# Kernel tuning notes

Hardware: AMD Instinct MI355X
Metric: run time of the kernel (lower is better)

## Reference

```python
import jax, jax.numpy as jnp
import numpy as np

D_IN = 64   # T (condition_length)
D = 128     # latent_dim
H = 8       # num_head
N = 2       # batch of graphs
M = 512     # num_nodes
T_OBS = 5.0


def leaky(v):
    return jnp.where(v >= 0, v, 0.2 * v)


def setup_inputs() -> dict:
    key = jax.random.key(0)
    ks = jax.random.split(key, 24)
    g = lambda k, s: jax.random.normal(k, s, dtype=jnp.float32) * 0.05
    return {
        "x": jax.random.normal(ks[0], (N, M, D_IN), dtype=jnp.float32),
        # f_node: T -> 2D -> D
        "fn_w1": g(ks[1], (D_IN, 2 * D)), "fn_b1": g(ks[2], (2 * D,)),
        "fn_w2": g(ks[3], (2 * D, D)),   "fn_b2": g(ks[4], (D,)),
        # per-head K/Q/V projections, stacked over heads
        "wk": g(ks[5], (H, D, D)), "bk": g(ks[6], (H, D)),
        "wq": g(ks[7], (H, D, D)), "bq": g(ks[8], (H, D)),
        "wv": g(ks[9], (H, D, D)), "bv": g(ks[10], (H, D)),
        # f_v: H*D -> D -> D
        "fv_w1": g(ks[11], (H * D, D)), "fv_b1": g(ks[12], (D,)),
        "fv_w2": g(ks[13], (D, D)),     "fv_b2": g(ks[14], (D,)),
        # f_node2edge: 2D -> D -> 1
        "fe_w1": g(ks[15], (2 * D, D)), "fe_b1": g(ks[16], (D,)),
        "fe_w2": g(ks[17], (D, 1)),     "fe_b2": g(ks[18], (1,)),
    }


def reference(x, fn_w1, fn_b1, fn_w2, fn_b2, wk, bk, wq, bq, wv, bv,
              fv_w1, fv_b1, fv_w2, fv_b2, fe_w1, fe_b1, fe_w2, fe_b2):
    n, m, T = x.shape
    # TemporalEncoding with d_hid=1: div_term = [1.0], even col -> sin(t)
    t = jnp.linspace(0.0, T_OBS, T)
    te = jnp.sin(t)  # [T]
    # f_node
    h = jax.nn.relu((x + te) @ fn_w1 + fn_b1) @ fn_w2 + fn_b2  # [N,M,D]
    # per-head attention (sender=K_i, receiver=Q_j -> scores = K Q^T)
    K = jnp.einsum('nmd,hde->hnme', h, wk) + bk[:, None, None, :]
    Q = jnp.einsum('nmd,hde->hnme', h, wq) + bq[:, None, None, :]
    V = jnp.einsum('nmd,hde->hnme', h, wv) + bv[:, None, None, :]
    scores = jnp.einsum('hnid,hnjd->hnij', K, Q)           # [H,N,M,M]
    alpha = jax.nn.softmax(leaky(scores), axis=-1)
    att = leaky(jnp.einsum('hnij,hnjd->hnid', alpha, V))   # [H,N,M,D]
    # concat heads along feature dim (head 0 first)
    att = jnp.transpose(att, (1, 2, 0, 3)).reshape(n, m, -1)  # [N,M,H*D]
    x2 = jax.nn.relu(att @ fv_w1 + fv_b1) @ fv_w2 + fv_b2 + h  # [N,M,D]
    # pairwise node2edge FFN: pair(i,j) = concat(x2_i, x2_j)
    half = fe_w1.shape[0] // 2
    A = x2 @ fe_w1[:half]   # contribution of node i
    B = x2 @ fe_w1[half:]   # contribution of node j
    hid = jax.nn.relu(A[:, :, None, :] + B[:, None, :, :] + fe_b1)  # [N,M,M,D]
    edge = (hid @ fe_w2 + fe_b2)[..., 0] / float(m)  # [N,M,M]
    return (x2, edge)
```

## Files before the change

### kernel.cpp

```cpp
#include <hip/hip_runtime.h>

typedef unsigned short u16;
typedef unsigned int u32;
typedef __attribute__((ext_vector_type(8))) short short8;
typedef __attribute__((ext_vector_type(4))) float f32x4;

__device__ __forceinline__ u16 f2b(float f) {
  union { float f; u32 i; } v; v.f = f;
  u32 i = v.i;
  return (u16)((i + 0x7FFFu + ((i >> 16) & 1u)) >> 16);
}
__device__ __forceinline__ float lo16(u32 x) { union { u32 i; float f; } v; v.i = x << 16; return v.f; }
__device__ __forceinline__ float hi16(u32 x) { union { u32 i; float f; } v; v.i = x & 0xffff0000u; return v.f; }
__device__ __forceinline__ u32 pack2(float a, float b) { return (u32)f2b(a) | ((u32)f2b(b) << 16); }

__device__ __align__(16) float g_h[1024 * 128];
__device__ __align__(16) u16   g_hb[1024 * 128];
__device__ __align__(16) u16   g_Wt[24 * 128 * 128];
__device__ __align__(16) u16   g_w1t[128 * 1024];
__device__ __align__(16) u16   g_K[16 * 512 * 128];
__device__ __align__(16) u16   g_Q[16 * 512 * 128];
__device__ __align__(16) u16   g_V[16 * 512 * 128];
__device__ __align__(16) u16   g_Opb[512 * 64 * 128];
__device__ __align__(16) float g_ml[512 * 64 * 2];
__device__ __align__(16) float g_part8[8 * 1024 * 128];
__device__ __align__(16) float g_A[1024 * 128];
__device__ __align__(16) float g_Bm[1024 * 128];

__global__ void k_fnode(const float* __restrict__ x, const float* __restrict__ w1,
                        const float* __restrict__ b1, const float* __restrict__ w2,
                        const float* __restrict__ b2, const float* __restrict__ wk,
                        const float* __restrict__ wq, const float* __restrict__ wv,
                        const float* __restrict__ fvw1) {
  __shared__ float xr[2 * 64];
  __shared__ float hids[2 * 256];
  __shared__ float red[2048];
  int tx = threadIdx.x;
  int row0 = blockIdx.x * 2;
  if (tx < 128) {
    int r = tx >> 6, k = tx & 63;
    xr[tx] = x[(row0 + r) * 64 + k] + sinf((float)k * (5.0f / 63.0f));
  }
  {
    int base = blockIdx.x * 1024 + tx;
#pragma unroll
    for (int t = 0; t < 4; t++) {
      int idx = base + t * 256;
      if (idx < 393216) {
        int ph = idx >> 14, rem = idx & 16383, e = rem >> 7, d = rem & 127;
        int proj = ph >> 3, head = ph & 7;
        const float* W = (proj == 0) ? wk : (proj == 1) ? wq : wv;
        g_Wt[idx] = f2b(W[head * 16384 + d * 128 + e]);
      } else {
        int idx2 = idx - 393216;
        int e = idx2 >> 10, k = idx2 & 1023;
        g_w1t[idx2] = f2b(fvw1[k * 128 + e]);
      }
    }
  }
  __syncthreads();
  {
    int ks = tx >> 6, cg = tx & 63;
    float acc[2][4] = {};
#pragma unroll 4
    for (int i = 0; i < 16; i++) {
      int k = ks * 16 + i;
      float4 w4 = *(const float4*)&w1[k * 256 + cg * 4];
      float a0 = xr[k], a1 = xr[64 + k];
      acc[0][0] = fmaf(a0, w4.x, acc[0][0]); acc[0][1] = fmaf(a0, w4.y, acc[0][1]);
      acc[0][2] = fmaf(a0, w4.z, acc[0][2]); acc[0][3] = fmaf(a0, w4.w, acc[0][3]);
      acc[1][0] = fmaf(a1, w4.x, acc[1][0]); acc[1][1] = fmaf(a1, w4.y, acc[1][1]);
      acc[1][2] = fmaf(a1, w4.z, acc[1][2]); acc[1][3] = fmaf(a1, w4.w, acc[1][3]);
    }
#pragma unroll
    for (int r = 0; r < 2; r++)
      *(float4*)&red[ks * 512 + r * 256 + cg * 4] = *(float4*)acc[r];
  }
  __syncthreads();
#pragma unroll
  for (int jo = 0; jo < 2; jo++) {
    int o = jo * 256 + tx;
    float s = red[o] + red[512 + o] + red[1024 + o] + red[1536 + o];
    hids[o] = fmaxf(s + b1[o & 255], 0.0f);
  }
  __syncthreads();
  {
    int ks = tx >> 5, eg = tx & 31;
    float acc[2][4] = {};
#pragma unroll 4
    for (int i = 0; i < 32; i++) {
      int k = ks * 32 + i;
      float4 w4 = *(const float4*)&w2[k * 128 + eg * 4];
      float a0 = hids[k], a1 = hids[256 + k];
      acc[0][0] = fmaf(a0, w4.x, acc[0][0]); acc[0][1] = fmaf(a0, w4.y, acc[0][1]);
      acc[0][2] = fmaf(a0, w4.z, acc[0][2]); acc[0][3] = fmaf(a0, w4.w, acc[0][3]);
      acc[1][0] = fmaf(a1, w4.x, acc[1][0]); acc[1][1] = fmaf(a1, w4.y, acc[1][1]);
      acc[1][2] = fmaf(a1, w4.z, acc[1][2]); acc[1][3] = fmaf(a1, w4.w, acc[1][3]);
    }
    __syncthreads();
#pragma unroll
    for (int r = 0; r < 2; r++)
      *(float4*)&red[ks * 256 + r * 128 + eg * 4] = *(float4*)acc[r];
  }
  __syncthreads();
  {
    float s = 0.0f;
#pragma unroll
    for (int ks = 0; ks < 8; ks++) s += red[ks * 256 + tx];
    int r = tx >> 7, e = tx & 127;
    float v = s + b2[e];
    g_h[(row0 + r) * 128 + e] = v;
    g_hb[(row0 + r) * 128 + e] = f2b(v);
  }
}

__global__ __launch_bounds__(256) void k_kqv(
    const float* __restrict__ bk, const float* __restrict__ bq,
    const float* __restrict__ bv) {
  __shared__ u16 hs[64 * 136];
  __shared__ u16 Wt[128 * 136];
  int b = blockIdx.x, tx = threadIdx.x;
  int rt = b & 15, ph = b >> 4;
  int proj = ph >> 3, head = ph & 7;
  const float* Bb = (proj == 0) ? bk : (proj == 1) ? bq : bv;
  u16* O = (proj == 0) ? g_K : (proj == 1) ? g_Q : g_V;
  int r0 = rt * 64;
#pragma unroll
  for (int t = 0; t < 4; t++) {
    int idx = t * 256 + tx, row = idx >> 4, oct = idx & 15;
    *(uint4*)&hs[row * 136 + oct * 8] = *(const uint4*)&g_hb[(r0 + row) * 128 + oct * 8];
  }
  const u16* Wtg = g_Wt + ph * 16384;
#pragma unroll
  for (int t = 0; t < 8; t++) {
    int idx = t * 256 + tx, row = idx >> 4, oct = idx & 15;
    *(uint4*)&Wt[row * 136 + oct * 8] = *(const uint4*)&Wtg[row * 128 + oct * 8];
  }
  __syncthreads();
  int lane = tx & 63, wv_ = tx >> 6, cl = lane & 15, quad = lane >> 4;
  short8 bH[4];
#pragma unroll
  for (int kk = 0; kk < 4; kk++)
    bH[kk] = *(const short8*)&hs[(wv_ * 16 + cl) * 136 + kk * 32 + quad * 8];
  f32x4 zero = {0.0f, 0.0f, 0.0f, 0.0f};
  f32x4 acc[8];
#pragma unroll
  for (int em = 0; em < 8; em++) acc[em] = zero;
#pragma unroll
  for (int em = 0; em < 8; em++)
#pragma unroll
    for (int kk = 0; kk < 4; kk++) {
      short8 aW = *(const short8*)&Wt[(em * 16 + cl) * 136 + kk * 32 + quad * 8];
      acc[em] = __builtin_amdgcn_mfma_f32_16x16x32_bf16(aW, bH[kk], acc[em], 0, 0, 0);
    }
#pragma unroll
  for (int em = 0; em < 8; em++) {
    float4 b4 = *(const float4*)&Bb[head * 128 + em * 16 + quad * 4];
    uint2 st = make_uint2(pack2(acc[em][0] + b4.x, acc[em][1] + b4.y),
                          pack2(acc[em][2] + b4.z, acc[em][3] + b4.w));
    *(uint2*)&O[(head * 1024 + r0 + wv_ * 16 + cl) * 128 + em * 16 + quad * 4] = st;
  }
}

__global__ __launch_bounds__(256) void k_attn() {
  __shared__ u16 Ks[64 * 136];
  __shared__ u16 Qs[64 * 136];
  __shared__ u16 Vt[128 * 72];
  __shared__ u16 Pw[4 * 16 * 72];
  __shared__ float alphas[4 * 16];
  int b = blockIdx.x, tx = threadIdx.x;
  int jc = b & 3, it = (b >> 2) & 7, hn = b >> 5;
  int i0 = it * 64;
  const u16* Kp = g_K + hn * 65536;
  const u16* Qp = g_Q + hn * 65536;
  const u16* Vp = g_V + hn * 65536;
#pragma unroll
  for (int t = 0; t < 4; t++) {
    int idx = t * 256 + tx, row = idx >> 4, oct = idx & 15;
    *(uint4*)&Ks[row * 136 + oct * 8] = *(const uint4*)&Kp[(i0 + row) * 128 + oct * 8];
  }
  int lane = tx & 63, wv = tx >> 6;
  int cl = lane & 15, quad = lane >> 4;
  f32x4 zero = {0.0f, 0.0f, 0.0f, 0.0f};
  f32x4 o[8];
#pragma unroll
  for (int es = 0; es < 8; es++) o[es] = zero;
  float m_ = -1e30f, l_ = 0.0f;

  for (int jt = 0; jt < 2; jt++) {
    int j0 = jc * 128 + jt * 64;
    __syncthreads();
#pragma unroll
    for (int t = 0; t < 4; t++) {
      int idx = t * 256 + tx, row = idx >> 4, oct = idx & 15;
      *(uint4*)&Qs[row * 136 + oct * 8] = *(const uint4*)&Qp[(j0 + row) * 128 + oct * 8];
    }
    {
      int jg = (tx & 15) * 4, e8 = (tx >> 4) * 8;
      uint4 r0 = *(const uint4*)&Vp[(j0 + jg + 0) * 128 + e8];
      uint4 r1 = *(const uint4*)&Vp[(j0 + jg + 1) * 128 + e8];
      uint4 r2 = *(const uint4*)&Vp[(j0 + jg + 2) * 128 + e8];
      uint4 r3 = *(const uint4*)&Vp[(j0 + jg + 3) * 128 + e8];
      const u32* p0 = (const u32*)&r0; const u32* p1 = (const u32*)&r1;
      const u32* p2 = (const u32*)&r2; const u32* p3 = (const u32*)&r3;
#pragma unroll
      for (int c = 0; c < 8; c++) {
        int w = c >> 1, sh = (c & 1) * 16;
        u32 lo = ((p0[w] >> sh) & 0xffffu) | (((p1[w] >> sh) & 0xffffu) << 16);
        u32 hi = ((p2[w] >> sh) & 0xffffu) | (((p3[w] >> sh) & 0xffffu) << 16);
        *(uint2*)&Vt[(e8 + c) * 72 + jg] = make_uint2(lo, hi);
      }
    }
    __syncthreads();
    short8 bK[4];
#pragma unroll
    for (int kk = 0; kk < 4; kk++)
      bK[kk] = *(const short8*)&Ks[(wv * 16 + cl) * 136 + kk * 32 + quad * 8];
    f32x4 st[4];
#pragma unroll
    for (int s = 0; s < 4; s++) {
      f32x4 acc = zero;
#pragma unroll
      for (int kk = 0; kk < 4; kk++) {
        short8 aQ = *(const short8*)&Qs[(s * 16 + cl) * 136 + kk * 32 + quad * 8];
        acc = __builtin_amdgcn_mfma_f32_16x16x32_bf16(aQ, bK[kk], acc, 0, 0, 0);
      }
      st[s] = acc;
    }
    float p[4][4];
    float tm = -1e30f;
#pragma unroll
    for (int s = 0; s < 4; s++)
#pragma unroll
      for (int r = 0; r < 4; r++) {
        float v = st[s][r];
        v = fmaxf(v, 0.2f * v);
        p[s][r] = v;
        tm = fmaxf(tm, v);
      }
    tm = fmaxf(tm, __shfl_xor(tm, 16));
    tm = fmaxf(tm, __shfl_xor(tm, 32));
    float mn = fmaxf(m_, tm);
    float alpha = __expf(m_ - mn);
    m_ = mn;
    float ps = 0.0f;
#pragma unroll
    for (int s = 0; s < 4; s++)
#pragma unroll
      for (int r = 0; r < 4; r++) {
        float e = __expf(p[s][r] - mn);
        p[s][r] = e;
        ps += e;
      }
    ps += __shfl_xor(ps, 16);
    ps += __shfl_xor(ps, 32);
    l_ = l_ * alpha + ps;
#pragma unroll
    for (int s = 0; s < 4; s++) {
      uint2 w2v = make_uint2(pack2(p[s][0], p[s][1]), pack2(p[s][2], p[s][3]));
      *(uint2*)&Pw[(wv * 16 + cl) * 72 + s * 16 + quad * 4] = w2v;
    }
    if (quad == 0) alphas[wv * 16 + cl] = alpha;
    __syncthreads();
    f32x4 av = *(const f32x4*)&alphas[wv * 16 + quad * 4];
#pragma unroll
    for (int es = 0; es < 8; es++) o[es] *= av;
    short8 aP[2];
#pragma unroll
    for (int k2 = 0; k2 < 2; k2++)
      aP[k2] = *(const short8*)&Pw[(wv * 16 + cl) * 72 + k2 * 32 + quad * 8];
#pragma unroll
    for (int es = 0; es < 8; es++) {
#pragma unroll
      for (int k2 = 0; k2 < 2; k2++) {
        short8 bV = *(const short8*)&Vt[(es * 16 + cl) * 72 + k2 * 32 + quad * 8];
        o[es] = __builtin_amdgcn_mfma_f32_16x16x32_bf16(aP[k2], bV, o[es], 0, 0, 0);
      }
    }
  }
#pragma unroll
  for (int es = 0; es < 8; es++)
#pragma unroll
    for (int r = 0; r < 4; r++)
      g_Opb[(b * 64 + wv * 16 + quad * 4 + r) * 128 + es * 16 + cl] = f2b(o[es][r]);
  if (quad == 0) {
    g_ml[(b * 64 + wv * 16 + cl) * 2 + 0] = m_;
    g_ml[(b * 64 + wv * 16 + cl) * 2 + 1] = l_;
  }
}

__global__ __launch_bounds__(256) void k_fv1() {
  __shared__ u16 atts[64 * 136];
  __shared__ u16 w1t[128 * 136];
  int b = blockIdx.x, tx = threadIdx.x;
  int kc = b & 7, rt = b >> 3;
  int r0 = rt * 64, k0 = kc * 128;
  int hn = kc * 2 + (rt >> 3), it = rt & 7;
#pragma unroll
  for (int t = 0; t < 8; t++) {
    int idx = t * 256 + tx, row = idx >> 4, oct = idx & 15;
    *(uint4*)&w1t[row * 136 + oct * 8] = *(const uint4*)&g_w1t[row * 1024 + k0 + oct * 8];
  }
  {
    int row = tx >> 2, cs = (tx & 3) * 32;
    float mc[4], lc[4];
#pragma unroll
    for (int c = 0; c < 4; c++) {
      float2 ml = *(const float2*)&g_ml[((hn * 32 + it * 4 + c) * 64 + row) * 2];
      mc[c] = ml.x; lc[c] = ml.y;
    }
    float ms = fmaxf(fmaxf(mc[0], mc[1]), fmaxf(mc[2], mc[3]));
    float lsum = 0.0f;
    float ra[32];
#pragma unroll
    for (int i = 0; i < 32; i++) ra[i] = 0.0f;
#pragma unroll
    for (int c = 0; c < 4; c++) {
      float w = __expf(mc[c] - ms);
      lsum += w * lc[c];
      const u16* src = &g_Opb[((hn * 32 + it * 4 + c) * 64 + row) * 128 + cs];
#pragma unroll
      for (int ov = 0; ov < 4; ov++) {
        uint4 v = *(const uint4*)&src[ov * 8];
        ra[ov * 8 + 0] = fmaf(w, lo16(v.x), ra[ov * 8 + 0]);
        ra[ov * 8 + 1] = fmaf(w, hi16(v.x), ra[ov * 8 + 1]);
        ra[ov * 8 + 2] = fmaf(w, lo16(v.y), ra[ov * 8 + 2]);
        ra[ov * 8 + 3] = fmaf(w, hi16(v.y), ra[ov * 8 + 3]);
        ra[ov * 8 + 4] = fmaf(w, lo16(v.z), ra[ov * 8 + 4]);
        ra[ov * 8 + 5] = fmaf(w, hi16(v.z), ra[ov * 8 + 5]);
        ra[ov * 8 + 6] = fmaf(w, lo16(v.w), ra[ov * 8 + 6]);
        ra[ov * 8 + 7] = fmaf(w, hi16(v.w), ra[ov * 8 + 7]);
      }
    }
    float inv = 1.0f / lsum;
    u32 pk[16];
#pragma unroll
    for (int i = 0; i < 16; i++) {
      float v0 = ra[i * 2] * inv;     v0 = fmaxf(v0, 0.2f * v0);
      float v1 = ra[i * 2 + 1] * inv; v1 = fmaxf(v1, 0.2f * v1);
      pk[i] = pack2(v0, v1);
    }
#pragma unroll
    for (int ov = 0; ov < 4; ov++)
      *(uint4*)&atts[row * 136 + cs + ov * 8] =
          make_uint4(pk[ov * 4], pk[ov * 4 + 1], pk[ov * 4 + 2], pk[ov * 4 + 3]);
  }
  __syncthreads();
  int lane = tx & 63, wv_ = tx >> 6, cl = lane & 15, quad = lane >> 4;
  short8 bA[4];
#pragma unroll
  for (int kk = 0; kk < 4; kk++)
    bA[kk] = *(const short8*)&atts[(wv_ * 16 + cl) * 136 + kk * 32 + quad * 8];
  f32x4 zero = {0.0f, 0.0f, 0.0f, 0.0f};
  f32x4 acc[8];
#pragma unroll
  for (int em = 0; em < 8; em++) acc[em] = zero;
#pragma unroll
  for (int em = 0; em < 8; em++)
#pragma unroll
    for (int kk = 0; kk < 4; kk++) {
      short8 aW = *(const short8*)&w1t[(em * 16 + cl) * 136 + kk * 32 + quad * 8];
      acc[em] = __builtin_amdgcn_mfma_f32_16x16x32_bf16(aW, bA[kk], acc[em], 0, 0, 0);
    }
#pragma unroll
  for (int em = 0; em < 8; em++)
    *(f32x4*)&g_part8[kc * 131072 + (r0 + wv_ * 16 + cl) * 128 + em * 16 + quad * 4] =
        acc[em];
}

__global__ void k_fv2(const float* __restrict__ b1, const float* __restrict__ w2,
                      const float* __restrict__ b2, const float* __restrict__ few1,
                      const float* __restrict__ feb1, float* __restrict__ x2out) {
  __shared__ float hids[2 * 128];
  __shared__ float x2s[2 * 128];
  __shared__ float red[8 * 256];
  int b = blockIdx.x, tx = threadIdx.x;
  int row0 = b * 2;
  {
    int r = tx >> 7, e = tx & 127;
    int gi = (row0 + r) * 128 + e;
    float s = b1[e];
#pragma unroll
    for (int kc = 0; kc < 8; kc++) s += g_part8[kc * 131072 + gi];
    hids[tx] = fmaxf(s, 0.0f);
  }
  __syncthreads();
  int ks = tx >> 5, eg = tx & 31;
  {
    float acc[2][4] = {};
#pragma unroll 4
    for (int i = 0; i < 16; i++) {
      int k = ks * 16 + i;
      float4 w4 = *(const float4*)&w2[k * 128 + eg * 4];
      float a0 = hids[k], a1 = hids[128 + k];
      acc[0][0] = fmaf(a0, w4.x, acc[0][0]); acc[0][1] = fmaf(a0, w4.y, acc[0][1]);
      acc[0][2] = fmaf(a0, w4.z, acc[0][2]); acc[0][3] = fmaf(a0, w4.w, acc[0][3]);
      acc[1][0] = fmaf(a1, w4.x, acc[1][0]); acc[1][1] = fmaf(a1, w4.y, acc[1][1]);
      acc[1][2] = fmaf(a1, w4.z, acc[1][2]); acc[1][3] = fmaf(a1, w4.w, acc[1][3]);
    }
#pragma unroll
    for (int r = 0; r < 2; r++)
      *(float4*)&red[ks * 256 + r * 128 + eg * 4] = *(float4*)acc[r];
  }
  __syncthreads();
  {
    float s = 0.0f;
#pragma unroll
    for (int k8 = 0; k8 < 8; k8++) s += red[k8 * 256 + tx];
    int r = tx >> 7, e = tx & 127;
    int gi = (row0 + r) * 128 + e;
    float c = s + b2[e] + g_h[gi];
    x2s[tx] = c;
    x2out[gi] = c;
  }
  __syncthreads();
  float aA[2][4] = {}, aB[2][4] = {};
#pragma unroll 4
  for (int i = 0; i < 16; i++) {
    int k = ks * 16 + i;
    float4 wa = *(const float4*)&few1[k * 128 + eg * 4];
    float4 wb = *(const float4*)&few1[(128 + k) * 128 + eg * 4];
    float a0 = x2s[k], a1 = x2s[128 + k];
    aA[0][0] = fmaf(a0, wa.x, aA[0][0]); aA[0][1] = fmaf(a0, wa.y, aA[0][1]);
    aA[0][2] = fmaf(a0, wa.z, aA[0][2]); aA[0][3] = fmaf(a0, wa.w, aA[0][3]);
    aA[1][0] = fmaf(a1, wa.x, aA[1][0]); aA[1][1] = fmaf(a1, wa.y, aA[1][1]);
    aA[1][2] = fmaf(a1, wa.z, aA[1][2]); aA[1][3] = fmaf(a1, wa.w, aA[1][3]);
    aB[0][0] = fmaf(a0, wb.x, aB[0][0]); aB[0][1] = fmaf(a0, wb.y, aB[0][1]);
    aB[0][2] = fmaf(a0, wb.z, aB[0][2]); aB[0][3] = fmaf(a0, wb.w, aB[0][3]);
    aB[1][0] = fmaf(a1, wb.x, aB[1][0]); aB[1][1] = fmaf(a1, wb.y, aB[1][1]);
    aB[1][2] = fmaf(a1, wb.z, aB[1][2]); aB[1][3] = fmaf(a1, wb.w, aB[1][3]);
  }
  __syncthreads();
#pragma unroll
  for (int r = 0; r < 2; r++)
    *(float4*)&red[ks * 256 + r * 128 + eg * 4] = *(float4*)aA[r];
  __syncthreads();
  {
    float s = 0.0f;
#pragma unroll
    for (int k8 = 0; k8 < 8; k8++) s += red[k8 * 256 + tx];
    int r = tx >> 7, e = tx & 127;
    g_A[(row0 + r) * 128 + e] = s + feb1[e];
  }
  __syncthreads();
#pragma unroll
  for (int r = 0; r < 2; r++)
    *(float4*)&red[ks * 256 + r * 128 + eg * 4] = *(float4*)aB[r];
  __syncthreads();
  {
    float s = 0.0f;
#pragma unroll
    for (int k8 = 0; k8 < 8; k8++) s += red[k8 * 256 + tx];
    int r = tx >> 7, e = tx & 127;
    g_Bm[(row0 + r) * 128 + e] = s;
  }
}

__global__ void k_edge(const float* __restrict__ few2, const float* __restrict__ feb2,
                       float* __restrict__ edge) {
  __shared__ float As[4 * 128];
  __shared__ float w2s[128];
  int b = blockIdx.x, tx = threadIdx.x;
  int n = b >> 8, rest = b & 255, ig = rest >> 1, jh = rest & 1;
  int i0 = ig * 4;
  if (tx < 128) w2s[tx] = few2[tx];
  As[tx] = g_A[(n * 512 + i0) * 128 + tx];
  As[tx + 256] = g_A[(n * 512 + i0) * 128 + tx + 256];
  float eb2 = feb2[0];
  __syncthreads();
  int j = jh * 256 + tx;
  const float* B0 = &g_Bm[(n * 512 + j) * 128];
  float acc[4] = {};
#pragma unroll 4
  for (int dc = 0; dc < 32; dc++) {
    float4 bv = *(const float4*)&B0[dc * 4];
    float4 w4 = *(const float4*)&w2s[dc * 4];
#pragma unroll
    for (int i = 0; i < 4; i++) {
      float4 a4 = *(const float4*)&As[i * 128 + dc * 4];
      acc[i] = fmaf(fmaxf(a4.x + bv.x, 0.0f), w4.x, acc[i]);
      acc[i] = fmaf(fmaxf(a4.y + bv.y, 0.0f), w4.y, acc[i]);
      acc[i] = fmaf(fmaxf(a4.z + bv.z, 0.0f), w4.z, acc[i]);
      acc[i] = fmaf(fmaxf(a4.w + bv.w, 0.0f), w4.w, acc[i]);
    }
  }
  const float scale = 1.0f / 512.0f;
#pragma unroll
  for (int i = 0; i < 4; i++)
    edge[(n * 512 + i0 + i) * 512 + j] = (acc[i] + eb2) * scale;
}

extern "C" void kernel_launch(void* const* d_in, const int* in_sizes, int n_in,
                              void* d_out, int out_size, void* d_ws, size_t ws_size,
                              hipStream_t stream) {
  (void)in_sizes; (void)n_in; (void)out_size; (void)d_ws; (void)ws_size;
  const float* x     = (const float*)d_in[0];
  const float* fn_w1 = (const float*)d_in[1];
  const float* fn_b1 = (const float*)d_in[2];
  const float* fn_w2 = (const float*)d_in[3];
  const float* fn_b2 = (const float*)d_in[4];
  const float* wk    = (const float*)d_in[5];
  const float* bk    = (const float*)d_in[6];
  const float* wq    = (const float*)d_in[7];
  const float* bq    = (const float*)d_in[8];
  const float* wv    = (const float*)d_in[9];
  const float* bv    = (const float*)d_in[10];
  const float* fv_w1 = (const float*)d_in[11];
  const float* fv_b1 = (const float*)d_in[12];
  const float* fv_w2 = (const float*)d_in[13];
  const float* fv_b2 = (const float*)d_in[14];
  const float* fe_w1 = (const float*)d_in[15];
  const float* fe_b1 = (const float*)d_in[16];
  const float* fe_w2 = (const float*)d_in[17];
  const float* fe_b2 = (const float*)d_in[18];

  float* x2out = (float*)d_out;
  float* edge  = x2out + 131072;

  k_fnode<<<512, 256, 0, stream>>>(x, fn_w1, fn_b1, fn_w2, fn_b2, wk, wq, wv, fv_w1);
  k_kqv<<<384, 256, 0, stream>>>(bk, bq, bv);
  k_attn<<<512, 256, 0, stream>>>();
  k_fv1<<<128, 256, 0, stream>>>();
  k_fv2<<<512, 256, 0, stream>>>(fv_b1, fv_w2, fv_b2, fe_w1, fe_b1, x2out);
  k_edge<<<512, 256, 0, stream>>>(fe_w2, fe_b2, edge);
}
```

Baseline: 143.1 us.

## Fuse six kernels into one cooperative persistent kernel with grid syncs

Merges the six stage kernels into a single cooperative kernel whose phases are separated by grid-wide syncs. Shared memory is a union sized for the largest phase, and the launch falls back to the separate kernels if the cooperative launch fails. The aim is to remove per-launch overhead and the gaps between the small kernels. In exchange the fused kernel is capped at two blocks per CU, and each grid sync costs something. The attention phase now reuses the K tile area for P and hoists the K fragment loads out of the j loop.

```diff
diff --git a/kernel.cpp b/kernel.cpp
--- a/kernel.cpp
+++ b/kernel.cpp
@@ -1,4 +1,7 @@
 #include <hip/hip_runtime.h>
+#include <hip/hip_cooperative_groups.h>
+
+namespace cg = cooperative_groups;
 
 typedef unsigned short u16;
 typedef unsigned int u32;
@@ -27,22 +30,33 @@
 __device__ __align__(16) float g_A[1024 * 128];
 __device__ __align__(16) float g_Bm[1024 * 128];
 
-__global__ void k_fnode(const float* __restrict__ x, const float* __restrict__ w1,
-                        const float* __restrict__ b1, const float* __restrict__ w2,
-                        const float* __restrict__ b2, const float* __restrict__ wk,
-                        const float* __restrict__ wq, const float* __restrict__ wv,
-                        const float* __restrict__ fvw1) {
-  __shared__ float xr[2 * 64];
-  __shared__ float hids[2 * 256];
-  __shared__ float red[2048];
-  int tx = threadIdx.x;
-  int row0 = blockIdx.x * 2;
+struct SM1 { float xr[128]; float hids[512]; float red[2048]; };
+struct SM2 { u16 hs[64 * 136]; u16 Wt[128 * 136]; };
+struct SM3 {
+  union { u16 Ks[64 * 136]; u16 Pw[64 * 72]; } kp;
+  u16 Qs[64 * 136];
+  u16 Vt[128 * 72];
+  float alphas[64];
+};
+struct SM4 { u16 atts[64 * 136]; u16 w1t[128 * 136]; };
+struct SM5 { float hids[256]; float x2s[256]; float red[2048]; };
+struct SM6 { float As[512]; float w2s[128]; };
+union __align__(16) SMem { SM1 p1; SM2 p2; SM3 p3; SM4 p4; SM5 p5; SM6 p6; };
+
+__device__ __forceinline__ void phase1(SM1& sm, int b, int tx,
+    const float* __restrict__ x, const float* __restrict__ fn_w1,
+    const float* __restrict__ fn_b1, const float* __restrict__ fn_w2,
+    const float* __restrict__ fn_b2, const float* __restrict__ wk,
+    const float* __restrict__ wq, const float* __restrict__ wv,
+    const float* __restrict__ fv_w1) {
+  __syncthreads();
+  int row0 = b * 2;
   if (tx < 128) {
     int r = tx >> 6, k = tx & 63;
-    xr[tx] = x[(row0 + r) * 64 + k] + sinf((float)k * (5.0f / 63.0f));
-  }
-  {
-    int base = blockIdx.x * 1024 + tx;
+    sm.xr[tx] = x[(row0 + r) * 64 + k] + sinf((float)k * (5.0f / 63.0f));
+  }
+  {
+    int base = b * 1024 + tx;
 #pragma unroll
     for (int t = 0; t < 4; t++) {
       int idx = base + t * 256;
@@ -54,19 +68,19 @@
       } else {
         int idx2 = idx - 393216;
         int e = idx2 >> 10, k = idx2 & 1023;
-        g_w1t[idx2] = f2b(fvw1[k * 128 + e]);
-      }
-    }
-  }
-  __syncthreads();
-  {
-    int ks = tx >> 6, cg = tx & 63;
+        g_w1t[idx2] = f2b(fv_w1[k * 128 + e]);
+      }
+    }
+  }
+  __syncthreads();
+  {
+    int ks = tx >> 6, cg_ = tx & 63;
     float acc[2][4] = {};
 #pragma unroll 4
     for (int i = 0; i < 16; i++) {
       int k = ks * 16 + i;
-      float4 w4 = *(const float4*)&w1[k * 256 + cg * 4];
-      float a0 = xr[k], a1 = xr[64 + k];
+      float4 w4 = *(const float4*)&fn_w1[k * 256 + cg_ * 4];
+      float a0 = sm.xr[k], a1 = sm.xr[64 + k];
       acc[0][0] = fmaf(a0, w4.x, acc[0][0]); acc[0][1] = fmaf(a0, w4.y, acc[0][1]);
       acc[0][2] = fmaf(a0, w4.z, acc[0][2]); acc[0][3] = fmaf(a0, w4.w, acc[0][3]);
       acc[1][0] = fmaf(a1, w4.x, acc[1][0]); acc[1][1] = fmaf(a1, w4.y, acc[1][1]);
@@ -74,14 +88,14 @@
     }
 #pragma unroll
     for (int r = 0; r < 2; r++)
-      *(float4*)&red[ks * 512 + r * 256 + cg * 4] = *(float4*)acc[r];
+      *(float4*)&sm.red[ks * 512 + r * 256 + cg_ * 4] = *(float4*)acc[r];
   }
   __syncthreads();
 #pragma unroll
   for (int jo = 0; jo < 2; jo++) {
     int o = jo * 256 + tx;
-    float s = red[o] + red[512 + o] + red[1024 + o] + red[1536 + o];
-    hids[o] = fmaxf(s + b1[o & 255], 0.0f);
+    float s = sm.red[o] + sm.red[512 + o] + sm.red[1024 + o] + sm.red[1536 + o];
+    sm.hids[o] = fmaxf(s + fn_b1[o & 255], 0.0f);
   }
   __syncthreads();
   {
@@ -90,8 +104,8 @@
 #pragma unroll 4
     for (int i = 0; i < 32; i++) {
       int k = ks * 32 + i;
-      float4 w4 = *(const float4*)&w2[k * 128 + eg * 4];
-      float a0 = hids[k], a1 = hids[256 + k];
+      float4 w4 = *(const float4*)&fn_w2[k * 128 + eg * 4];
+      float a0 = sm.hids[k], a1 = sm.hids[256 + k];
       acc[0][0] = fmaf(a0, w4.x, acc[0][0]); acc[0][1] = fmaf(a0, w4.y, acc[0][1]);
       acc[0][2] = fmaf(a0, w4.z, acc[0][2]); acc[0][3] = fmaf(a0, w4.w, acc[0][3]);
       acc[1][0] = fmaf(a1, w4.x, acc[1][0]); acc[1][1] = fmaf(a1, w4.y, acc[1][1]);
@@ -100,26 +114,24 @@
     __syncthreads();
 #pragma unroll
     for (int r = 0; r < 2; r++)
-      *(float4*)&red[ks * 256 + r * 128 + eg * 4] = *(float4*)acc[r];
+      *(float4*)&sm.red[ks * 256 + r * 128 + eg * 4] = *(float4*)acc[r];
   }
   __syncthreads();
   {
     float s = 0.0f;
 #pragma unroll
-    for (int ks = 0; ks < 8; ks++) s += red[ks * 256 + tx];
+    for (int ks = 0; ks < 8; ks++) s += sm.red[ks * 256 + tx];
     int r = tx >> 7, e = tx & 127;
-    float v = s + b2[e];
+    float v = s + fn_b2[e];
     g_h[(row0 + r) * 128 + e] = v;
     g_hb[(row0 + r) * 128 + e] = f2b(v);
   }
 }
 
-__global__ __launch_bounds__(256) void k_kqv(
+__device__ __forceinline__ void phase2(SM2& sm, int b, int tx,
     const float* __restrict__ bk, const float* __restrict__ bq,
     const float* __restrict__ bv) {
-  __shared__ u16 hs[64 * 136];
-  __shared__ u16 Wt[128 * 136];
-  int b = blockIdx.x, tx = threadIdx.x;
+  __syncthreads();
   int rt = b & 15, ph = b >> 4;
   int proj = ph >> 3, head = ph & 7;
   const float* Bb = (proj == 0) ? bk : (proj == 1) ? bq : bv;
@@ -128,20 +140,20 @@
 #pragma unroll
   for (int t = 0; t < 4; t++) {
     int idx = t * 256 + tx, row = idx >> 4, oct = idx & 15;
-    *(uint4*)&hs[row * 136 + oct * 8] = *(const uint4*)&g_hb[(r0 + row) * 128 + oct * 8];
+    *(uint4*)&sm.hs[row * 136 + oct * 8] = *(const uint4*)&g_hb[(r0 + row) * 128 + oct * 8];
   }
   const u16* Wtg = g_Wt + ph * 16384;
 #pragma unroll
   for (int t = 0; t < 8; t++) {
     int idx = t * 256 + tx, row = idx >> 4, oct = idx & 15;
-    *(uint4*)&Wt[row * 136 + oct * 8] = *(const uint4*)&Wtg[row * 128 + oct * 8];
+    *(uint4*)&sm.Wt[row * 136 + oct * 8] = *(const uint4*)&Wtg[row * 128 + oct * 8];
   }
   __syncthreads();
   int lane = tx & 63, wv_ = tx >> 6, cl = lane & 15, quad = lane >> 4;
   short8 bH[4];
 #pragma unroll
   for (int kk = 0; kk < 4; kk++)
-    bH[kk] = *(const short8*)&hs[(wv_ * 16 + cl) * 136 + kk * 32 + quad * 8];
+    bH[kk] = *(const short8*)&sm.hs[(wv_ * 16 + cl) * 136 + kk * 32 + quad * 8];
   f32x4 zero = {0.0f, 0.0f, 0.0f, 0.0f};
   f32x4 acc[8];
 #pragma unroll
@@ -150,7 +162,7 @@
   for (int em = 0; em < 8; em++)
 #pragma unroll
     for (int kk = 0; kk < 4; kk++) {
-      short8 aW = *(const short8*)&Wt[(em * 16 + cl) * 136 + kk * 32 + quad * 8];
+      short8 aW = *(const short8*)&sm.Wt[(em * 16 + cl) * 136 + kk * 32 + quad * 8];
       acc[em] = __builtin_amdgcn_mfma_f32_16x16x32_bf16(aW, bH[kk], acc[em], 0, 0, 0);
     }
 #pragma unroll
@@ -162,13 +174,8 @@
   }
 }
 
-__global__ __launch_bounds__(256) void k_attn() {
-  __shared__ u16 Ks[64 * 136];
-  __shared__ u16 Qs[64 * 136];
-  __shared__ u16 Vt[128 * 72];
-  __shared__ u16 Pw[4 * 16 * 72];
-  __shared__ float alphas[4 * 16];
-  int b = blockIdx.x, tx = threadIdx.x;
+__device__ __forceinline__ void phase3(SM3& sm, int b, int tx) {
+  __syncthreads();
   int jc = b & 3, it = (b >> 2) & 7, hn = b >> 5;
   int i0 = it * 64;
   const u16* Kp = g_K + hn * 65536;
@@ -177,10 +184,15 @@
 #pragma unroll
   for (int t = 0; t < 4; t++) {
     int idx = t * 256 + tx, row = idx >> 4, oct = idx & 15;
-    *(uint4*)&Ks[row * 136 + oct * 8] = *(const uint4*)&Kp[(i0 + row) * 128 + oct * 8];
-  }
-  int lane = tx & 63, wv = tx >> 6;
+    *(uint4*)&sm.kp.Ks[row * 136 + oct * 8] = *(const uint4*)&Kp[(i0 + row) * 128 + oct * 8];
+  }
+  __syncthreads();
+  int lane = tx & 63, wvx = tx >> 6;
   int cl = lane & 15, quad = lane >> 4;
+  short8 bK[4];
+#pragma unroll
+  for (int kk = 0; kk < 4; kk++)
+    bK[kk] = *(const short8*)&sm.kp.Ks[(wvx * 16 + cl) * 136 + kk * 32 + quad * 8];
   f32x4 zero = {0.0f, 0.0f, 0.0f, 0.0f};
   f32x4 o[8];
 #pragma unroll
@@ -193,7 +205,7 @@
 #pragma unroll
     for (int t = 0; t < 4; t++) {
       int idx = t * 256 + tx, row = idx >> 4, oct = idx & 15;
-      *(uint4*)&Qs[row * 136 + oct * 8] = *(const uint4*)&Qp[(j0 + row) * 128 + oct * 8];
+      *(uint4*)&sm.Qs[row * 136 + oct * 8] = *(const uint4*)&Qp[(j0 + row) * 128 + oct * 8];
     }
     {
       int jg = (tx & 15) * 4, e8 = (tx >> 4) * 8;
@@ -208,21 +220,17 @@
         int w = c >> 1, sh = (c & 1) * 16;
         u32 lo = ((p0[w] >> sh) & 0xffffu) | (((p1[w] >> sh) & 0xffffu) << 16);
         u32 hi = ((p2[w] >> sh) & 0xffffu) | (((p3[w] >> sh) & 0xffffu) << 16);
-        *(uint2*)&Vt[(e8 + c) * 72 + jg] = make_uint2(lo, hi);
+        *(uint2*)&sm.Vt[(e8 + c) * 72 + jg] = make_uint2(lo, hi);
       }
     }
     __syncthreads();
-    short8 bK[4];
-#pragma unroll
-    for (int kk = 0; kk < 4; kk++)
-      bK[kk] = *(const short8*)&Ks[(wv * 16 + cl) * 136 + kk * 32 + quad * 8];
     f32x4 st[4];
 #pragma unroll
     for (int s = 0; s < 4; s++) {
       f32x4 acc = zero;
 #pragma unroll
       for (int kk = 0; kk < 4; kk++) {
-        short8 aQ = *(const short8*)&Qs[(s * 16 + cl) * 136 + kk * 32 + quad * 8];
+        short8 aQ = *(const short8*)&sm.Qs[(s * 16 + cl) * 136 + kk * 32 + quad * 8];
         acc = __builtin_amdgcn_mfma_f32_16x16x32_bf16(aQ, bK[kk], acc, 0, 0, 0);
       }
       st[s] = acc;
@@ -258,22 +266,22 @@
 #pragma unroll
     for (int s = 0; s < 4; s++) {
       uint2 w2v = make_uint2(pack2(p[s][0], p[s][1]), pack2(p[s][2], p[s][3]));
-      *(uint2*)&Pw[(wv * 16 + cl) * 72 + s * 16 + quad * 4] = w2v;
-    }
-    if (quad == 0) alphas[wv * 16 + cl] = alpha;
+      *(uint2*)&sm.kp.Pw[(wvx * 16 + cl) * 72 + s * 16 + quad * 4] = w2v;
+    }
+    if (quad == 0) sm.alphas[wvx * 16 + cl] = alpha;
     __syncthreads();
-    f32x4 av = *(const f32x4*)&alphas[wv * 16 + quad * 4];
+    f32x4 av = *(const f32x4*)&sm.alphas[wvx * 16 + quad * 4];
 #pragma unroll
     for (int es = 0; es < 8; es++) o[es] *= av;
     short8 aP[2];
 #pragma unroll
     for (int k2 = 0; k2 < 2; k2++)
-      aP[k2] = *(const short8*)&Pw[(wv * 16 + cl) * 72 + k2 * 32 + quad * 8];
+      aP[k2] = *(const short8*)&sm.kp.Pw[(wvx * 16 + cl) * 72 + k2 * 32 + quad * 8];
 #pragma unroll
     for (int es = 0; es < 8; es++) {
 #pragma unroll
       for (int k2 = 0; k2 < 2; k2++) {
-        short8 bV = *(const short8*)&Vt[(es * 16 + cl) * 72 + k2 * 32 + quad * 8];
+        short8 bV = *(const short8*)&sm.Vt[(es * 16 + cl) * 72 + k2 * 32 + quad * 8];
         o[es] = __builtin_amdgcn_mfma_f32_16x16x32_bf16(aP[k2], bV, o[es], 0, 0, 0);
       }
     }
@@ -282,24 +290,22 @@
   for (int es = 0; es < 8; es++)
 #pragma unroll
     for (int r = 0; r < 4; r++)
-      g_Opb[(b * 64 + wv * 16 + quad * 4 + r) * 128 + es * 16 + cl] = f2b(o[es][r]);
+      g_Opb[(b * 64 + wvx * 16 + quad * 4 + r) * 128 + es * 16 + cl] = f2b(o[es][r]);
   if (quad == 0) {
-    g_ml[(b * 64 + wv * 16 + cl) * 2 + 0] = m_;
-    g_ml[(b * 64 + wv * 16 + cl) * 2 + 1] = l_;
-  }
-}
-
-__global__ __launch_bounds__(256) void k_fv1() {
-  __shared__ u16 atts[64 * 136];
-  __shared__ u16 w1t[128 * 136];
-  int b = blockIdx.x, tx = threadIdx.x;
+    g_ml[(b * 64 + wvx * 16 + cl) * 2 + 0] = m_;
+    g_ml[(b * 64 + wvx * 16 + cl) * 2 + 1] = l_;
+  }
+}
+
+__device__ __forceinline__ void phase4(SM4& sm, int b, int tx) {
+  __syncthreads();
   int kc = b & 7, rt = b >> 3;
   int r0 = rt * 64, k0 = kc * 128;
   int hn = kc * 2 + (rt >> 3), it = rt & 7;
 #pragma unroll
   for (int t = 0; t < 8; t++) {
     int idx = t * 256 + tx, row = idx >> 4, oct = idx & 15;
-    *(uint4*)&w1t[row * 136 + oct * 8] = *(const uint4*)&g_w1t[row * 1024 + k0 + oct * 8];
+    *(uint4*)&sm.w1t[row * 136 + oct * 8] = *(const uint4*)&g_w1t[row * 1024 + k0 + oct * 8];
   }
   {
     int row = tx >> 2, cs = (tx & 3) * 32;
@@ -342,7 +348,7 @@
     }
 #pragma unroll
     for (int ov = 0; ov < 4; ov++)
-      *(uint4*)&atts[row * 136 + cs + ov * 8] =
+      *(uint4*)&sm.atts[row * 136 + cs + ov * 8] =
           make_uint4(pk[ov * 4], pk[ov * 4 + 1], pk[ov * 4 + 2], pk[ov * 4 + 3]);
   }
   __syncthreads();
@@ -350,7 +356,7 @@
   short8 bA[4];
 #pragma unroll
   for (int kk = 0; kk < 4; kk++)
-    bA[kk] = *(const short8*)&atts[(wv_ * 16 + cl) * 136 + kk * 32 + quad * 8];
+    bA[kk] = *(const short8*)&sm.atts[(wv_ * 16 + cl) * 136 + kk * 32 + quad * 8];
   f32x4 zero = {0.0f, 0.0f, 0.0f, 0.0f};
   f32x4 acc[8];
 #pragma unroll
@@ -359,7 +365,7 @@
   for (int em = 0; em < 8; em++)
 #pragma unroll
     for (int kk = 0; kk < 4; kk++) {
-      short8 aW = *(const short8*)&w1t[(em * 16 + cl) * 136 + kk * 32 + quad * 8];
+      short8 aW = *(const short8*)&sm.w1t[(em * 16 + cl) * 136 + kk * 32 + quad * 8];
       acc[em] = __builtin_amdgcn_mfma_f32_16x16x32_bf16(aW, bA[kk], acc[em], 0, 0, 0);
     }
 #pragma unroll
@@ -368,21 +374,19 @@
         acc[em];
 }
 
-__global__ void k_fv2(const float* __restrict__ b1, const float* __restrict__ w2,
-                      const float* __restrict__ b2, const float* __restrict__ few1,
-                      const float* __restrict__ feb1, float* __restrict__ x2out) {
-  __shared__ float hids[2 * 128];
-  __shared__ float x2s[2 * 128];
-  __shared__ float red[8 * 256];
-  int b = blockIdx.x, tx = threadIdx.x;
+__device__ __forceinline__ void phase5(SM5& sm, int b, int tx,
+    const float* __restrict__ fv_b1, const float* __restrict__ fv_w2,
+    const float* __restrict__ fv_b2, const float* __restrict__ fe_w1,
+    const float* __restrict__ fe_b1, float* __restrict__ x2out) {
+  __syncthreads();
   int row0 = b * 2;
   {
     int r = tx >> 7, e = tx & 127;
     int gi = (row0 + r) * 128 + e;
-    float s = b1[e];
+    float s = fv_b1[e];
 #pragma unroll
     for (int kc = 0; kc < 8; kc++) s += g_part8[kc * 131072 + gi];
-    hids[tx] = fmaxf(s, 0.0f);
+    sm.hids[tx] = fmaxf(s, 0.0f);
   }
   __syncthreads();
   int ks = tx >> 5, eg = tx & 31;
@@ -391,8 +395,8 @@
 #pragma unroll 4
     for (int i = 0; i < 16; i++) {
       int k = ks * 16 + i;
-      float4 w4 = *(const float4*)&w2[k * 128 + eg * 4];
-      float a0 = hids[k], a1 = hids[128 + k];
+      float4 w4 = *(const float4*)&fv_w2[k * 128 + eg * 4];
+      float a0 = sm.hids[k], a1 = sm.hids[128 + k];
       acc[0][0] = fmaf(a0, w4.x, acc[0][0]); acc[0][1] = fmaf(a0, w4.y, acc[0][1]);
       acc[0][2] = fmaf(a0, w4.z, acc[0][2]); acc[0][3] = fmaf(a0, w4.w, acc[0][3]);
       acc[1][0] = fmaf(a1, w4.x, acc[1][0]); acc[1][1] = fmaf(a1, w4.y, acc[1][1]);
@@ -400,17 +404,17 @@
     }
 #pragma unroll
     for (int r = 0; r < 2; r++)
-      *(float4*)&red[ks * 256 + r * 128 + eg * 4] = *(float4*)acc[r];
+      *(float4*)&sm.red[ks * 256 + r * 128 + eg * 4] = *(float4*)acc[r];
   }
   __syncthreads();
   {
     float s = 0.0f;
 #pragma unroll
-    for (int k8 = 0; k8 < 8; k8++) s += red[k8 * 256 + tx];
+    for (int k8 = 0; k8 < 8; k8++) s += sm.red[k8 * 256 + tx];
     int r = tx >> 7, e = tx & 127;
     int gi = (row0 + r) * 128 + e;
-    float c = s + b2[e] + g_h[gi];
-    x2s[tx] = c;
+    float c = s + fv_b2[e] + g_h[gi];
+    sm.x2s[tx] = c;
     x2out[gi] = c;
   }
   __syncthreads();
@@ -418,9 +422,9 @@
 #pragma unroll 4
   for (int i = 0; i < 16; i++) {
     int k = ks * 16 + i;
-    float4 wa = *(const float4*)&few1[k * 128 + eg * 4];
-    float4 wb = *(const float4*)&few1[(128 + k) * 128 + eg * 4];
-    float a0 = x2s[k], a1 = x2s[128 + k];
+    float4 wa = *(const float4*)&fe_w1[k * 128 + eg * 4];
+    float4 wb = *(const float4*)&fe_w1[(128 + k) * 128 + eg * 4];
+    float a0 = sm.x2s[k], a1 = sm.x2s[128 + k];
     aA[0][0] = fmaf(a0, wa.x, aA[0][0]); aA[0][1] = fmaf(a0, wa.y, aA[0][1]);
     aA[0][2] = fmaf(a0, wa.z, aA[0][2]); aA[0][3] = fmaf(a0, wa.w, aA[0][3]);
     aA[1][0] = fmaf(a1, wa.x, aA[1][0]); aA[1][1] = fmaf(a1, wa.y, aA[1][1]);
@@ -433,61 +437,119 @@
   __syncthreads();
 #pragma unroll
   for (int r = 0; r < 2; r++)
-    *(float4*)&red[ks * 256 + r * 128 + eg * 4] = *(float4*)aA[r];
+    *(float4*)&sm.red[ks * 256 + r * 128 + eg * 4] = *(float4*)aA[r];
   __syncthreads();
   {
     float s = 0.0f;
 #pragma unroll
-    for (int k8 = 0; k8 < 8; k8++) s += red[k8 * 256 + tx];
+    for (int k8 = 0; k8 < 8; k8++) s += sm.red[k8 * 256 + tx];
     int r = tx >> 7, e = tx & 127;
-    g_A[(row0 + r) * 128 + e] = s + feb1[e];
+    g_A[(row0 + r) * 128 + e] = s + fe_b1[e];
   }
   __syncthreads();
 #pragma unroll
   for (int r = 0; r < 2; r++)
-    *(float4*)&red[ks * 256 + r * 128 + eg * 4] = *(float4*)aB[r];
+    *(float4*)&sm.red[ks * 256 + r * 128 + eg * 4] = *(float4*)aB[r];
   __syncthreads();
   {
     float s = 0.0f;
 #pragma unroll
-    for (int k8 = 0; k8 < 8; k8++) s += red[k8 * 256 + tx];
+    for (int k8 = 0; k8 < 8; k8++) s += sm.red[k8 * 256 + tx];
     int r = tx >> 7, e = tx & 127;
     g_Bm[(row0 + r) * 128 + e] = s;
   }
 }
 
-__global__ void k_edge(const float* __restrict__ few2, const float* __restrict__ feb2,
-                       float* __restrict__ edge) {
-  __shared__ float As[4 * 128];
-  __shared__ float w2s[128];
-  int b = blockIdx.x, tx = threadIdx.x;
+__device__ __forceinline__ void phase6(SM6& sm, int b, int tx,
+    const float* __restrict__ fe_w2, const float* __restrict__ fe_b2,
+    float* __restrict__ edge) {
+  __syncthreads();
   int n = b >> 8, rest = b & 255, ig = rest >> 1, jh = rest & 1;
   int i0 = ig * 4;
-  if (tx < 128) w2s[tx] = few2[tx];
-  As[tx] = g_A[(n * 512 + i0) * 128 + tx];
-  As[tx + 256] = g_A[(n * 512 + i0) * 128 + tx + 256];
-  float eb2 = feb2[0];
+  if (tx < 128) sm.w2s[tx] = fe_w2[tx];
+  sm.As[tx] = g_A[(n * 512 + i0) * 128 + tx];
+  sm.As[tx + 256] = g_A[(n * 512 + i0) * 128 + tx + 256];
+  float eb2 = fe_b2[0];
   __syncthreads();
   int j = jh * 256 + tx;
   const float* B0 = &g_Bm[(n * 512 + j) * 128];
   float acc[4] = {};
 #pragma unroll 4
   for (int dc = 0; dc < 32; dc++) {
-    float4 bv = *(const float4*)&B0[dc * 4];
-    float4 w4 = *(const float4*)&w2s[dc * 4];
+    float4 bv4 = *(const float4*)&B0[dc * 4];
+    float4 w4 = *(const float4*)&sm.w2s[dc * 4];
 #pragma unroll
     for (int i = 0; i < 4; i++) {
-      float4 a4 = *(const float4*)&As[i * 128 + dc * 4];
-      acc[i] = fmaf(fmaxf(a4.x + bv.x, 0.0f), w4.x, acc[i]);
-      acc[i] = fmaf(fmaxf(a4.y + bv.y, 0.0f), w4.y, acc[i]);
-      acc[i] = fmaf(fmaxf(a4.z + bv.z, 0.0f), w4.z, acc[i]);
-      acc[i] = fmaf(fmaxf(a4.w + bv.w, 0.0f), w4.w, acc[i]);
+      float4 a4 = *(const float4*)&sm.As[i * 128 + dc * 4];
+      acc[i] = fmaf(fmaxf(a4.x + bv4.x, 0.0f), w4.x, acc[i]);
+      acc[i] = fmaf(fmaxf(a4.y + bv4.y, 0.0f), w4.y, acc[i]);
+      acc[i] = fmaf(fmaxf(a4.z + bv4.z, 0.0f), w4.z, acc[i]);
+      acc[i] = fmaf(fmaxf(a4.w + bv4.w, 0.0f), w4.w, acc[i]);
     }
   }
   const float scale = 1.0f / 512.0f;
 #pragma unroll
   for (int i = 0; i < 4; i++)
     edge[(n * 512 + i0 + i) * 512 + j] = (acc[i] + eb2) * scale;
+}
+
+__global__ __launch_bounds__(256, 2) void k_fused(
+    const float* __restrict__ x, const float* __restrict__ fn_w1,
+    const float* __restrict__ fn_b1, const float* __restrict__ fn_w2,
+    const float* __restrict__ fn_b2, const float* __restrict__ wk,
+    const float* __restrict__ bk, const float* __restrict__ wq,
+    const float* __restrict__ bq, const float* __restrict__ wv,
+    const float* __restrict__ bv, const float* __restrict__ fv_w1,
+    const float* __restrict__ fv_b1, const float* __restrict__ fv_w2,
+    const float* __restrict__ fv_b2, const float* __restrict__ fe_w1,
+    const float* __restrict__ fe_b1, const float* __restrict__ fe_w2,
+    const float* __restrict__ fe_b2, float* __restrict__ x2out,
+    float* __restrict__ edge) {
+  __shared__ SMem sm;
+  cg::grid_group grid = cg::this_grid();
+  int b = blockIdx.x, tx = threadIdx.x, G = gridDim.x;
+  for (int vb = b; vb < 512; vb += G)
+    phase1(sm.p1, vb, tx, x, fn_w1, fn_b1, fn_w2, fn_b2, wk, wq, wv, fv_w1);
+  grid.sync();
+  for (int vb = b; vb < 384; vb += G) phase2(sm.p2, vb, tx, bk, bq, bv);
+  grid.sync();
+  for (int vb = b; vb < 512; vb += G) phase3(sm.p3, vb, tx);
+  grid.sync();
+  for (int vb = b; vb < 128; vb += G) phase4(sm.p4, vb, tx);
+  grid.sync();
+  for (int vb = b; vb < 512; vb += G)
+    phase5(sm.p5, vb, tx, fv_b1, fv_w2, fv_b2, fe_w1, fe_b1, x2out);
+  grid.sync();
+  for (int vb = b; vb < 512; vb += G) phase6(sm.p6, vb, tx, fe_w2, fe_b2, edge);
+}
+
+__global__ void k1(const float* x, const float* w1, const float* b1,
+                   const float* w2, const float* b2, const float* wk,
+                   const float* wq, const float* wv, const float* fvw1) {
+  __shared__ SM1 s;
+  phase1(s, blockIdx.x, threadIdx.x, x, w1, b1, w2, b2, wk, wq, wv, fvw1);
+}
+__global__ __launch_bounds__(256) void k2(const float* bk, const float* bq,
+                                          const float* bv) {
+  __shared__ SM2 s;
+  phase2(s, blockIdx.x, threadIdx.x, bk, bq, bv);
+}
+__global__ __launch_bounds__(256) void k3() {
+  __shared__ SM3 s;
+  phase3(s, blockIdx.x, threadIdx.x);
+}
+__global__ __launch_bounds__(256) void k4() {
+  __shared__ SM4 s;
+  phase4(s, blockIdx.x, threadIdx.x);
+}
+__global__ void k5(const float* b1, const float* w2, const float* b2,
+                   const float* few1, const float* feb1, float* x2out) {
+  __shared__ SM5 s;
+  phase5(s, blockIdx.x, threadIdx.x, b1, w2, b2, few1, feb1, x2out);
+}
+__global__ void k6(const float* few2, const float* feb2, float* edge) {
+  __shared__ SM6 s;
+  phase6(s, blockIdx.x, threadIdx.x, few2, feb2, edge);
 }
 
 extern "C" void kernel_launch(void* const* d_in, const int* in_sizes, int n_in,
@@ -517,10 +579,47 @@
   float* x2out = (float*)d_out;
   float* edge  = x2out + 131072;
 
-  k_fnode<<<512, 256, 0, stream>>>(x, fn_w1, fn_b1, fn_w2, fn_b2, wk, wq, wv, fv_w1);
-  k_kqv<<<384, 256, 0, stream>>>(bk, bq, bv);
-  k_attn<<<512, 256, 0, stream>>>();
-  k_fv1<<<128, 256, 0, stream>>>();
-  k_fv2<<<512, 256, 0, stream>>>(fv_b1, fv_w2, fv_b2, fe_w1, fe_b1, x2out);
-  k_edge<<<512, 256, 0, stream>>>(fe_w2, fe_b2, edge);
-}
+  static int mode = 0;
+
+  if (mode >= 0) {
+    void* args[] = {
+        (void*)&x,     (void*)&fn_w1, (void*)&fn_b1, (void*)&fn_w2, (void*)&fn_b2,
+        (void*)&wk,    (void*)&bk,    (void*)&wq,    (void*)&bq,    (void*)&wv,
+        (void*)&bv,    (void*)&fv_w1, (void*)&fv_b1, (void*)&fv_w2, (void*)&fv_b2,
+        (void*)&fe_w1, (void*)&fe_b1, (void*)&fe_w2, (void*)&fe_b2, (void*)&x2out,
+        (void*)&edge};
+    if (mode > 0) {
+      if (hipLaunchCooperativeKernel((const void*)k_fused, dim3(mode), dim3(256),
+                                     args, 0, stream) == hipSuccess)
+        return;
+      (void)hipGetLastError();
+      mode = -1;
+    } else {
+      int nb = 0;
+      if (hipOccupancyMaxActiveBlocksPerMultiprocessor(
+              &nb, (const void*)k_fused, 256, 0) != hipSuccess)
+        nb = 0;
+      (void)hipGetLastError();
+      int cands[2];
+      int nc = 0;
+      if (nb >= 2) cands[nc++] = 512;
+      cands[nc++] = 256;
+      for (int t = 0; t < nc; t++) {
+        if (hipLaunchCooperativeKernel((const void*)k_fused, dim3(cands[t]),
+                                       dim3(256), args, 0, stream) == hipSuccess) {
+          mode = cands[t];
+          return;
+        }
+        (void)hipGetLastError();
+      }
+      mode = -1;
+    }
+  }
+
+  k1<<<512, 256, 0, stream>>>(x, fn_w1, fn_b1, fn_w2, fn_b2, wk, wq, wv, fv_w1);
+  k2<<<384, 256, 0, stream>>>(bk, bq, bv);
+  k3<<<512, 256, 0, stream>>>();
+  k4<<<128, 256, 0, stream>>>();
+  k5<<<512, 256, 0, stream>>>(fv_b1, fv_w2, fv_b2, fe_w1, fe_b1, x2out);
+  k6<<<512, 256, 0, stream>>>(fe_w2, fe_b2, edge);
+}
```

Result: slower. 341.2 us (+138.5%).
